# Optimization experiments

Measured on AMD Instinct MI355X. Metric: run time of the kernel, lower is better.

## Reference

```python
import math
import jax, jax.numpy as jnp
import numpy as np

TAU = 2.0 * math.pi
# First 32 imaginary parts of non-trivial zeta zeros (n_pairs = d_head//2 = 32)
RIEMANN_ZEROS_IM = (
    14.134725142, 21.022039639, 25.01085758, 30.424876126, 32.935061588,
    37.586178159, 40.918719012, 43.327073281, 48.005150881, 49.773832478,
    52.970321478, 56.446247697, 59.347044003, 60.831778525, 65.112544048,
    67.079810529, 69.546401711, 72.067157674, 75.704690699, 77.144840069,
    79.33737502, 82.910380854, 84.735492981, 87.425274613, 88.809111208,
    92.491899271, 94.651344041, 95.870634228, 98.831194218, 101.317851006,
    103.72553804, 105.446623052,
)

B, N, D_MODEL, N_HEADS = 2, 2048, 512, 8


def setup_inputs() -> dict:
    key = jax.random.key(0)
    k1, k2, k3 = jax.random.split(key, 3)
    d = D_MODEL
    x = jax.random.normal(k1, (B, N, d), dtype=jnp.float32)
    # scale weights ~ Xavier so attention logits stay in a sane range
    w_qkv = jax.random.normal(k2, (d, 3 * d), dtype=jnp.float32) * (d ** -0.5)
    w_o = jax.random.normal(k3, (d, d), dtype=jnp.float32) * (d ** -0.5)
    log_scale = jnp.zeros((N_HEADS,), dtype=jnp.float32)
    log_lambda_sigma = jnp.zeros((N_HEADS,), dtype=jnp.float32)
    return {"x": x, "w_qkv": w_qkv, "w_o": w_o,
            "log_scale": log_scale, "log_lambda_sigma": log_lambda_sigma}


def _rotate_pairs(t, cos, sin):
    # t: (B,H,N,dh); cos/sin: (H,N,K) with K = dh//2; rotate adjacent dim pairs
    t1 = t[..., 0::2]
    t2 = t[..., 1::2]
    c = cos[None]
    s = sin[None]
    r1 = t1 * c - t2 * s
    r2 = t1 * s + t2 * c
    return jnp.stack([r1, r2], axis=-1).reshape(t.shape)


def reference(x, w_qkv, w_o, log_scale, log_lambda_sigma):
    b, n, d_model = x.shape
    h = log_scale.shape[0]
    dh = d_model // h
    kpairs = dh // 2

    # qkv projection and head split
    qkv = (x @ w_qkv).reshape(b, n, 3, h, dh)
    q = jnp.transpose(qkv[:, :, 0], (0, 2, 1, 3))  # (B,H,N,dh)
    k = jnp.transpose(qkv[:, :, 1], (0, 2, 1, 3))
    v = jnp.transpose(qkv[:, :, 2], (0, 2, 1, 3))

    # phase theta(h,p,k) = log1p(p) * gamma_k * exp(log_scale_h)
    gamma = jnp.asarray(RIEMANN_ZEROS_IM[:kpairs], dtype=jnp.float32)
    gamma = gamma / gamma[0]  # normalize_gamma
    tau_t = jnp.log1p(jnp.arange(n, dtype=jnp.float32))
    theta = (tau_t[None, :, None] * gamma[None, None, :]
             * jnp.exp(log_scale)[:, None, None])  # (H,N,K)
    cos, sin = jnp.cos(theta), jnp.sin(theta)

    # sheet index sigma = floor(theta / 2pi); int cast in torch kills grad
    sheet = jax.lax.stop_gradient(jnp.floor(theta / TAU))  # (H,N,K) float

    # mean cross-pair |sigma_i - sigma_j|, accumulated over K via scan so the
    # (H,N,N,K) diff tensor never materializes (mirrors the module's tiling)
    def body(acc, sk):  # sk: (H,N)
        return acc + jnp.abs(sk[:, :, None] - sk[:, None, :]), None
    mean_abs, _ = jax.lax.scan(body, jnp.zeros((h, n, n), dtype=jnp.float32),
                               jnp.moveaxis(sheet, -1, 0))
    mean_abs = mean_abs / kpairs  # (H,N,N)

    lam = jnp.exp(log_lambda_sigma)  # (H,)
    sheet_bias = -lam[:, None, None] * mean_abs  # (H,N,N)
    causal = jnp.tril(jnp.ones((n, n), dtype=bool))
    bias = jnp.where(causal[None], sheet_bias, -jnp.inf)  # (H,N,N)

    q_rot = _rotate_pairs(q, cos, sin)
    k_rot = _rotate_pairs(k, cos, sin)

    scores = jnp.einsum("bhqd,bhkd->bhqk", q_rot, k_rot) / math.sqrt(dh)
    scores = scores + bias[None]
    attn = jax.nn.softmax(scores, axis=-1)
    out = jnp.einsum("bhqk,bhkd->bhqd", attn, v)
    out = jnp.transpose(out, (0, 2, 1, 3)).reshape(b, n, d_model)
    return out @ w_o
```

## Files before the change

kernel.cpp:

```cpp
#include <hip/hip_runtime.h>
#include <hip/hip_bf16.h>
#include <math.h>

#define NSEQ 2048
#define NH 8
#define DH 64
#define KP 32
#define DM 512
#define NB 2
#define MROWS (NB * NSEQ)
#define SLOT4 144

typedef short bf16x8 __attribute__((ext_vector_type(8)));
typedef float f32x4  __attribute__((ext_vector_type(4)));

static __constant__ float RZF[KP] = {
    14.134725142f, 21.022039639f, 25.01085758f,  30.424876126f, 32.935061588f,
    37.586178159f, 40.918719012f, 43.327073281f, 48.005150881f, 49.773832478f,
    52.970321478f, 56.446247697f, 59.347044003f, 60.831778525f, 65.112544048f,
    67.079810529f, 69.546401711f, 72.067157674f, 75.704690699f, 77.144840069f,
    79.33737502f,  82.910380854f, 84.735492981f, 87.425274613f, 88.809111208f,
    92.491899271f, 94.651344041f, 95.870634228f, 98.831194218f, 101.317851006f,
    103.72553804f, 105.446623052f};

static __device__ __forceinline__ unsigned short f2bf(float f) {
    unsigned int u = __float_as_uint(f);
    unsigned int r = (u + 0x7FFFu + ((u >> 16) & 1u)) >> 16;
    return (unsigned short)r;
}
static __device__ __forceinline__ float bf2f(unsigned short s) {
    return __uint_as_float((unsigned int)s << 16);
}

static __device__ __forceinline__ void gload16(const void* g, void* l) {
    __builtin_amdgcn_global_load_lds(
        (const __attribute__((address_space(1))) void*)g,
        (__attribute__((address_space(3))) void*)l, 16, 0, 0);
}

__global__ __launch_bounds__(256) void k_prep(
    const float* __restrict__ x, const float* __restrict__ wq,
    const float* __restrict__ wo, const float* __restrict__ ls,
    const float* __restrict__ ll,
    unsigned short* __restrict__ xb, unsigned short* __restrict__ wqT,
    unsigned short* __restrict__ woT,
    float* __restrict__ cosT, float* __restrict__ sinT, float* __restrict__ biasK)
{
    __shared__ float tile[32][33];
    int bid = blockIdx.x;
    int tid = threadIdx.x;
    if (bid < 1024) {
        int i = bid * 256 + tid;
        float4 a = ((const float4*)x)[2 * i];
        float4 b = ((const float4*)x)[2 * i + 1];
        union { unsigned short s[8]; uint4 u; } pk;
        pk.s[0] = f2bf(a.x); pk.s[1] = f2bf(a.y); pk.s[2] = f2bf(a.z); pk.s[3] = f2bf(a.w);
        pk.s[4] = f2bf(b.x); pk.s[5] = f2bf(b.y); pk.s[6] = f2bf(b.z); pk.s[7] = f2bf(b.w);
        ((uint4*)xb)[i] = pk.u;
    } else if (bid < 2048) {
        const float* src; unsigned short* dst; int R, C, bx, by;
        if (bid < 1792) { src = wq; dst = wqT; R = DM; C = 3 * DM;
                          int ix = bid - 1024; bx = ix % 48; by = ix / 48; }
        else            { src = wo; dst = woT; R = DM; C = DM;
                          int ix = bid - 1792; bx = ix & 15; by = ix >> 4; }
        int x0 = bx << 5, y0 = by << 5;
        int tx = tid & 31, ty = tid >> 5;
#pragma unroll
        for (int i = 0; i < 4; ++i)
            tile[ty + i * 8][tx] = src[(size_t)(y0 + ty + i * 8) * C + x0 + tx];
        __syncthreads();
#pragma unroll
        for (int i = 0; i < 4; ++i)
            dst[(size_t)(x0 + ty + i * 8) * R + y0 + tx] = f2bf(tile[tx][ty + i * 8]);
    } else {
        int item = (bid - 2048) * 256 + tid;
        int p   = item & 31;
        int idx = item >> 5;
        int h = idx >> 11;
        int t = idx & (NSEQ - 1);
        float scale = expf(ls[h]);
        float tau = log1pf((float)t);
        const float TAUF = 6.2831853071795864769f;
        float g  = RZF[p] / RZF[0];
        float th = (tau * g) * scale;
        cosT[(size_t)idx * KP + p] = cosf(th);
        sinT[(size_t)idx * KP + p] = sinf(th);
        float fl = floorf(th / TAUF);
        fl += __shfl_xor(fl, 1);
        fl += __shfl_xor(fl, 2);
        fl += __shfl_xor(fl, 4);
        fl += __shfl_xor(fl, 8);
        fl += __shfl_xor(fl, 16);
        if (p == 0) biasK[idx] = expf(ll[h]) * (1.0f / 32.0f) * fl;
    }
}

__global__ __launch_bounds__(256) void k_gemm_qkv(
    const unsigned short* __restrict__ xb, const unsigned short* __restrict__ wt,
    const float* __restrict__ cosT, const float* __restrict__ sinT,
    unsigned short* __restrict__ qrot, unsigned short* __restrict__ krot,
    unsigned short* __restrict__ vtout)
{
    __shared__ char Asm[2][64 * 128];
    __shared__ char Bsm[2][128 * 128];
    int tid = threadIdx.x;
    int w = tid >> 6, lane = tid & 63, g = lane >> 4, c = lane & 15;
    int wm = w >> 1, wn = w & 1;
    int bm = blockIdx.y << 6, bn = blockIdx.x << 7;
    int rin = lane >> 3;
    int csw = ((lane & 7) ^ rin) << 4;

    f32x4 acc[2][4];
#pragma unroll
    for (int mi = 0; mi < 2; ++mi)
#pragma unroll
        for (int ni = 0; ni < 4; ++ni) acc[mi][ni] = (f32x4){0.f, 0.f, 0.f, 0.f};

    const char* Ag = (const char*)xb;
    const char* Bg = (const char*)wt;

    auto stage = [&](int buf, int k0) {
#pragma unroll
        for (int ch = 0; ch < 2; ++ch) {
            int chA = w * 2 + ch;
            int row = chA * 8 + rin;
            gload16(Ag + ((size_t)(bm + row) * DM + k0) * 2 + csw, Asm[buf] + chA * 1024);
        }
#pragma unroll
        for (int ch = 0; ch < 4; ++ch) {
            int chB = w * 4 + ch;
            int row = chB * 8 + rin;
            gload16(Bg + ((size_t)(bn + row) * DM + k0) * 2 + csw, Bsm[buf] + chB * 1024);
        }
    };

    stage(0, 0);
    asm volatile("s_waitcnt vmcnt(0)" ::: "memory");
    __syncthreads();
    int cur = 0;

    for (int k0 = 0; k0 < DM; k0 += 64) {
        if (k0 + 64 < DM) stage(cur ^ 1, k0 + 64);
#pragma unroll
        for (int kk = 0; kk < 2; ++kk) {
            bf16x8 af[2], bfr[4];
#pragma unroll
            for (int mi = 0; mi < 2; ++mi) {
                int row = wm * 32 + mi * 16 + c;
                af[mi] = *(const bf16x8*)(Asm[cur] + ((row * 128 + kk * 64 + g * 16) ^ ((row & 7) << 4)));
            }
#pragma unroll
            for (int ni = 0; ni < 4; ++ni) {
                int row = wn * 64 + ni * 16 + c;
                bfr[ni] = *(const bf16x8*)(Bsm[cur] + ((row * 128 + kk * 64 + g * 16) ^ ((row & 7) << 4)));
            }
#pragma unroll
            for (int mi = 0; mi < 2; ++mi)
#pragma unroll
                for (int ni = 0; ni < 4; ++ni)
                    acc[mi][ni] = __builtin_amdgcn_mfma_f32_16x16x32_bf16(
                        af[mi], bfr[ni], acc[mi][ni], 0, 0, 0);
        }
        asm volatile("s_waitcnt vmcnt(0)" ::: "memory");
        __syncthreads();
        cur ^= 1;
    }

    int lane_odd = c & 1;
#pragma unroll
    for (int ni = 0; ni < 4; ++ni) {
        int n = bn + wn * 64 + ni * 16 + c;
        int sec = n >> 9;
        int dmod = n & 511;
        int h = dmod >> 6, dh = dmod & 63, p = dh >> 1;
        if (sec == 2) {
#pragma unroll
            for (int mi = 0; mi < 2; ++mi) {
                int m0 = bm + wm * 32 + mi * 16 + g * 4;
                int b = m0 >> 11, t0 = m0 & (NSEQ - 1);
                union { unsigned short s[4]; uint2 u; } pk;
                pk.s[0] = f2bf(acc[mi][ni][0]); pk.s[1] = f2bf(acc[mi][ni][1]);
                pk.s[2] = f2bf(acc[mi][ni][2]); pk.s[3] = f2bf(acc[mi][ni][3]);
                *(uint2*)(vtout + ((size_t)(b * NH + h) * DH + dh) * NSEQ + t0) = pk.u;
            }
        } else {
            const float* cb_ = cosT + (size_t)h * NSEQ * KP + p;
            const float* sb_ = sinT + (size_t)h * NSEQ * KP + p;
            unsigned short* dst = (sec == 0) ? qrot : krot;
            float osc = (sec == 0) ? 0.125f : 1.0f;
#pragma unroll
            for (int mi = 0; mi < 2; ++mi) {
#pragma unroll
                for (int r = 0; r < 4; ++r) {
                    int m = bm + wm * 32 + mi * 16 + g * 4 + r;
                    int b = m >> 11, t = m & (NSEQ - 1);
                    float val = acc[mi][ni][r];
                    float pv = __shfl_xor(val, 1);
                    float cv = cb_[(size_t)t * KP], sv = sb_[(size_t)t * KP];
                    float o = lane_odd ? (pv * sv + val * cv) : (val * cv - pv * sv);
                    dst[((size_t)(b * NH + h) * NSEQ + t) * DH + dh] = f2bf(o * osc);
                }
            }
        }
    }
}

__global__ __launch_bounds__(256) void k_attn(
    const unsigned short* __restrict__ qr, const unsigned short* __restrict__ kr,
    const unsigned short* __restrict__ vt, const float* __restrict__ biasK,
    unsigned short* __restrict__ ao, unsigned short* __restrict__ opart,
    float* __restrict__ mlpart)
{
    __shared__ char Kbuf[8192];
    __shared__ char Vbuf[8192];
    __shared__ char Pl[4][2048];
    __shared__ float Bk[64];

    int bid = blockIdx.x;
    int xcd = bid & 7;
    int i   = bid >> 3;
    int bh  = xcd * 2 + (i & 1);
    int slot = (SLOT4 - 1) - (i >> 1);
    int b = bh >> 3, h = bh & 7;
    int s = slot, qt = 0, nch;
    for (;;) { nch = (qt + 4) >> 2; if (s < nch) break; s -= nch; ++qt; }
    int ci = s;
    int t0 = ci << 2;
    int t1 = min(t0 + 4, qt + 1);

    int q0 = qt << 6;
    int tid = threadIdx.x;
    int w    = tid >> 6;
    int lane = tid & 63;
    int g    = lane >> 4;
    int c    = lane & 15;
    char* Pb = Pl[w];

    const char* kb  = (const char*)(kr + (size_t)bh * NSEQ * DH);
    const char* vtb = (const char*)(vt + (size_t)bh * DH * NSEQ);
    const unsigned short* qb = qr + (size_t)bh * NSEQ * DH;
    const float* bkrow = biasK + (size_t)h * NSEQ;

    int qg = q0 + (w << 4) + c;

    bf16x8 qf[2];
#pragma unroll
    for (int sl = 0; sl < 2; ++sl)
        qf[sl] = *(const bf16x8*)(qb + (size_t)qg * DH + sl * 32 + g * 8);

    f32x4 oa[4];
#pragma unroll
    for (int dt = 0; dt < 4; ++dt) oa[dt] = (f32x4){0.f, 0.f, 0.f, 0.f};
    float mr = -3.0e38f, lr = 0.0f;

    int rin = lane >> 3;
    int swz = ((lane & 7) ^ rin) << 4;

    for (int tile = t0; tile < t1; ++tile) {
        int j0 = tile << 6;
#pragma unroll
        for (int ii = 0; ii < 2; ++ii) {
            int ch = w * 2 + ii;
            int row = ch * 8 + rin;
            gload16(kb  + (size_t)(j0 + row) * 128 + swz, Kbuf + ch * 1024);
            gload16(vtb + (size_t)row * (NSEQ * 2) + (size_t)j0 * 2 + swz,
                    Vbuf + ch * 1024);
        }
        if (tid < 64) Bk[tid] = bkrow[j0 + tid];
        asm volatile("s_waitcnt vmcnt(0)" ::: "memory");
        __syncthreads();

        f32x4 st[4];
#pragma unroll
        for (int kt = 0; kt < 4; ++kt) st[kt] = (f32x4){0.f, 0.f, 0.f, 0.f};
#pragma unroll
        for (int sl = 0; sl < 2; ++sl) {
#pragma unroll
            for (int kt = 0; kt < 4; ++kt) {
                int row = kt * 16 + c;
                bf16x8 af = *(const bf16x8*)(Kbuf +
                    ((row * 128 + sl * 64 + g * 16) ^ ((row & 7) << 4)));
                st[kt] = __builtin_amdgcn_mfma_f32_16x16x32_bf16(af, qf[sl], st[kt], 0, 0, 0);
            }
        }

        bool diagT = (tile == qt);
        float sv[16];
#pragma unroll
        for (int kt = 0; kt < 4; ++kt) {
#pragma unroll
            for (int r4 = 0; r4 < 4; ++r4) {
                int ki = kt * 16 + g * 4 + r4;
                float vl = st[kt][r4] + Bk[ki];
                if (diagT && (j0 + ki > qg)) vl = -3.0e38f;
                sv[kt * 4 + r4] = vl;
            }
        }

        float m16 = sv[0];
#pragma unroll
        for (int ii = 1; ii < 16; ++ii) m16 = fmaxf(m16, sv[ii]);
        m16 = fmaxf(m16, __shfl_xor(m16, 16));
        m16 = fmaxf(m16, __shfl_xor(m16, 32));
        if (__any(m16 > mr + 8.0f)) {
            float mt = fmaxf(mr, m16);
            float corr = __expf(mr - mt);
            mr = mt;
            lr *= corr;
            float corrO[4];
#pragma unroll
            for (int r4 = 0; r4 < 4; ++r4) corrO[r4] = __shfl(corr, g * 4 + r4);
#pragma unroll
            for (int dt = 0; dt < 4; ++dt)
#pragma unroll
                for (int r4 = 0; r4 < 4; ++r4) oa[dt][r4] *= corrO[r4];
        }
        float psum = 0.0f;
        unsigned int pw[8];
#pragma unroll
        for (int ii = 0; ii < 8; ++ii) {
            float p0 = __expf(sv[2 * ii]     - mr);
            float p1 = __expf(sv[2 * ii + 1] - mr);
            psum += p0 + p1;
            asm("v_cvt_pk_bf16_f32 %0, %1, %2" : "=v"(pw[ii]) : "v"(p0), "v"(p1));
        }
        lr += psum;

#pragma unroll
        for (int kt = 0; kt < 4; ++kt) {
            uint2 u2; u2.x = pw[2 * kt]; u2.y = pw[2 * kt + 1];
            *(uint2*)(Pb + ((c * 128 + kt * 32 + g * 8) ^ ((c & 7) << 4))) = u2;
        }

#pragma unroll
        for (int sl = 0; sl < 2; ++sl) {
            bf16x8 pa = *(const bf16x8*)(Pb + ((c * 128 + sl * 64 + g * 16) ^ ((c & 7) << 4)));
#pragma unroll
            for (int dt = 0; dt < 4; ++dt) {
                int d = dt * 16 + c;
                bf16x8 vf = *(const bf16x8*)(Vbuf +
                    ((d * 128 + sl * 64 + g * 16) ^ ((d & 7) << 4)));
                oa[dt] = __builtin_amdgcn_mfma_f32_16x16x32_bf16(pa, vf, oa[dt], 0, 0, 0);
            }
        }
        __syncthreads();
    }

    lr += __shfl_xor(lr, 16);
    lr += __shfl_xor(lr, 32);
    if (nch == 1) {
        float inv = 1.0f / lr;
        float invO[4];
#pragma unroll
        for (int r4 = 0; r4 < 4; ++r4) invO[r4] = __shfl(inv, g * 4 + r4);
#pragma unroll
        for (int dt = 0; dt < 4; ++dt)
#pragma unroll
            for (int r4 = 0; r4 < 4; ++r4) {
                int row = q0 + (w << 4) + g * 4 + r4;
                ao[((size_t)b * NSEQ + row) * DM + h * DH + dt * 16 + c] =
                    f2bf(oa[dt][r4] * invO[r4]);
            }
    } else {
        size_t obase = ((size_t)bh * SLOT4 + slot) * (64 * 64);
#pragma unroll
        for (int dt = 0; dt < 4; ++dt)
#pragma unroll
            for (int r4 = 0; r4 < 4; ++r4) {
                int row = (w << 4) + g * 4 + r4;
                opart[obase + row * 64 + dt * 16 + c] = f2bf(oa[dt][r4]);
            }
        if (g == 0) {
            size_t mb = (((size_t)bh * SLOT4 + slot) * 64 + (w << 4) + c) * 2;
            mlpart[mb]     = mr;
            mlpart[mb + 1] = lr;
        }
    }
}

__global__ __launch_bounds__(256) void k_merge(
    const unsigned short* __restrict__ opart, const float* __restrict__ mlpart,
    unsigned short* __restrict__ ao)
{
    int bh = blockIdx.y;
    int b = bh >> 3, h = bh & 7;
    int qt = 4 + blockIdx.x;
    int nch = (qt + 4) >> 2;
    int slot0 = 0;
    for (int q = 0; q < qt; ++q) slot0 += (q + 4) >> 2;
    int tid = threadIdx.x;
    int row = tid >> 2;
    int d0 = (tid & 3) << 4;

    size_t pbase = ((size_t)bh * SLOT4 + slot0) * 4096 + row * 64 + d0;
    size_t mbase = (((size_t)bh * SLOT4 + slot0) * 64 + row) * 2;

    float M = -3.0e38f;
#pragma unroll
    for (int cc = 0; cc < 8; ++cc)
        if (cc < nch) M = fmaxf(M, mlpart[mbase + (size_t)cc * 128]);

    float L = 0.0f;
    float o[16];
#pragma unroll
    for (int ii = 0; ii < 16; ++ii) o[ii] = 0.0f;
#pragma unroll
    for (int cc = 0; cc < 8; ++cc) {
        if (cc < nch) {
            float mc = mlpart[mbase + (size_t)cc * 128];
            float lc = mlpart[mbase + (size_t)cc * 128 + 1];
            float wgt = __expf(mc - M);
            L += lc * wgt;
            union { uint4 u; unsigned short sh[8]; } lo, hi;
            lo.u = *(const uint4*)(opart + pbase + (size_t)cc * 4096);
            hi.u = *(const uint4*)(opart + pbase + (size_t)cc * 4096 + 8);
#pragma unroll
            for (int ii = 0; ii < 8; ++ii) {
                o[ii]     += bf2f(lo.sh[ii]) * wgt;
                o[ii + 8] += bf2f(hi.sh[ii]) * wgt;
            }
        }
    }
    float invL = 1.0f / L;
    int grow = (qt << 6) + row;
    unsigned short* dst = ao + ((size_t)b * NSEQ + grow) * DM + h * DH + d0;
    union { unsigned short sh[8]; uint4 u; } p0, p1;
#pragma unroll
    for (int ii = 0; ii < 8; ++ii) {
        p0.sh[ii] = f2bf(o[ii] * invL);
        p1.sh[ii] = f2bf(o[ii + 8] * invL);
    }
    *(uint4*)dst = p0.u;
    *(uint4*)(dst + 8) = p1.u;
}

__global__ __launch_bounds__(256) void k_gemm_out(
    const unsigned short* __restrict__ aob, const unsigned short* __restrict__ wt,
    float* __restrict__ out)
{
    __shared__ char Asm[64 * 128];
    __shared__ char Bsm[64 * 128];
    int tid = threadIdx.x;
    int w = tid >> 6, lane = tid & 63, g = lane >> 4, c = lane & 15;
    int wm = w >> 1, wn = w & 1;
    int bm = blockIdx.y << 6, bn = blockIdx.x << 6;
    int rin = lane >> 3;
    int csw = ((lane & 7) ^ rin) << 4;

    f32x4 acc[2][2];
#pragma unroll
    for (int mi = 0; mi < 2; ++mi)
#pragma unroll
        for (int ni = 0; ni < 2; ++ni) acc[mi][ni] = (f32x4){0.f, 0.f, 0.f, 0.f};

    const char* Ag = (const char*)aob;
    const char* Bg = (const char*)wt;

    for (int k0 = 0; k0 < DM; k0 += 64) {
        __syncthreads();
#pragma unroll
        for (int ch = 0; ch < 2; ++ch) {
            int chA = w * 2 + ch;
            int row = chA * 8 + rin;
            gload16(Ag + ((size_t)(bm + row) * DM + k0) * 2 + csw, Asm + chA * 1024);
        }
#pragma unroll
        for (int ch = 0; ch < 2; ++ch) {
            int chB = w * 2 + ch;
            int row = chB * 8 + rin;
            gload16(Bg + ((size_t)(bn + row) * DM + k0) * 2 + csw, Bsm + chB * 1024);
        }
        asm volatile("s_waitcnt vmcnt(0)" ::: "memory");
        __syncthreads();
#pragma unroll
        for (int kk = 0; kk < 2; ++kk) {
            bf16x8 af[2], bfr[2];
#pragma unroll
            for (int mi = 0; mi < 2; ++mi) {
                int row = wm * 32 + mi * 16 + c;
                af[mi] = *(const bf16x8*)(Asm + ((row * 128 + kk * 64 + g * 16) ^ ((row & 7) << 4)));
            }
#pragma unroll
            for (int ni = 0; ni < 2; ++ni) {
                int row = wn * 32 + ni * 16 + c;
                bfr[ni] = *(const bf16x8*)(Bsm + ((row * 128 + kk * 64 + g * 16) ^ ((row & 7) << 4)));
            }
#pragma unroll
            for (int mi = 0; mi < 2; ++mi)
#pragma unroll
                for (int ni = 0; ni < 2; ++ni)
                    acc[mi][ni] = __builtin_amdgcn_mfma_f32_16x16x32_bf16(
                        af[mi], bfr[ni], acc[mi][ni], 0, 0, 0);
        }
    }

#pragma unroll
    for (int ni = 0; ni < 2; ++ni) {
        int n = bn + wn * 32 + ni * 16 + c;
#pragma unroll
        for (int mi = 0; mi < 2; ++mi)
#pragma unroll
            for (int r = 0; r < 4; ++r) {
                int m = bm + wm * 32 + mi * 16 + g * 4 + r;
                out[(size_t)m * DM + n] = acc[mi][ni][r];
            }
    }
}

extern "C" void kernel_launch(void* const* d_in, const int* in_sizes, int n_in,
                              void* d_out, int out_size, void* d_ws, size_t ws_size,
                              hipStream_t stream)
{
    const float* x  = (const float*)d_in[0];
    const float* wq = (const float*)d_in[1];
    const float* wo = (const float*)d_in[2];
    const float* ls = (const float*)d_in[3];
    const float* ll = (const float*)d_in[4];
    float* out = (float*)d_out;

    char* ws = (char*)d_ws;
    size_t off = 0;
    float* cosT  = (float*)(ws + off); off += (size_t)NH * NSEQ * KP * 4;
    float* sinT  = (float*)(ws + off); off += (size_t)NH * NSEQ * KP * 4;
    float* biasK = (float*)(ws + off); off += (size_t)NH * NSEQ * 4;
    unsigned short* xb  = (unsigned short*)(ws + off); off += (size_t)MROWS * DM * 2;
    unsigned short* wqT = (unsigned short*)(ws + off); off += (size_t)DM * 3 * DM * 2;
    unsigned short* woT = (unsigned short*)(ws + off); off += (size_t)DM * DM * 2;
    unsigned short* qbf = (unsigned short*)(ws + off); off += (size_t)MROWS * DM * 2;
    unsigned short* kbf = (unsigned short*)(ws + off); off += (size_t)MROWS * DM * 2;
    unsigned short* vtb = (unsigned short*)(ws + off); off += (size_t)MROWS * DM * 2;
    unsigned short* aob = (unsigned short*)(ws + off); off += (size_t)MROWS * DM * 2;
    unsigned short* opart = (unsigned short*)(ws + off);
    off += (size_t)NB * NH * SLOT4 * 64 * 64 * 2;
    float* mlpart = (float*)(ws + off); off += (size_t)NB * NH * SLOT4 * 64 * 2 * 4;

    k_prep<<<4096, 256, 0, stream>>>(x, wq, wo, ls, ll, xb, wqT, woT, cosT, sinT, biasK);
    k_gemm_qkv<<<dim3(3 * DM / 128, MROWS / 64), 256, 0, stream>>>(
        xb, wqT, cosT, sinT, qbf, kbf, vtb);
    k_attn<<<8 * 288, 256, 0, stream>>>(
        qbf, kbf, vtb, biasK, aob, opart, mlpart);
    k_merge<<<dim3(28, NB * NH), 256, 0, stream>>>(opart, mlpart, aob);
    k_gemm_out<<<dim3(DM / 64, MROWS / 64), 256, 0, stream>>>(aob, woT, out);
}
```

Before: 71.07 us.

## Fold log2e into scores, use raw v_exp, load V directly into registers

Folds the log2(e) factor into the Q scaling and the sheet bias, so the softmax and merge steps can call the hardware base-2 exponential directly instead of __expf. V fragments are now loaded from global memory straight into registers, which removes the V shared-memory buffer and the LDS round trip. The kernel gets a launch-bounds occupancy hint, and the lazy-rescale threshold is raised to match the base-2 domain. In exchange, each wave now issues its own V global loads, which cost more bandwidth than the shared async copy did, and register pressure rises.

```diff
diff --git a/kernel.cpp b/kernel.cpp
--- a/kernel.cpp
+++ b/kernel.cpp
@@ -10,6 +10,7 @@
 #define NB 2
 #define MROWS (NB * NSEQ)
 #define SLOT4 144
+#define LOG2E 1.4426950408889634f
 
 typedef short bf16x8 __attribute__((ext_vector_type(8)));
 typedef float f32x4  __attribute__((ext_vector_type(4)));
@@ -30,6 +31,9 @@
 }
 static __device__ __forceinline__ float bf2f(unsigned short s) {
     return __uint_as_float((unsigned int)s << 16);
+}
+static __device__ __forceinline__ float exp2q(float x) {
+    float r; asm("v_exp_f32 %0, %1" : "=v"(r) : "v"(x)); return r;
 }
 
 static __device__ __forceinline__ void gload16(const void* g, void* l) {
@@ -91,7 +95,7 @@
         fl += __shfl_xor(fl, 4);
         fl += __shfl_xor(fl, 8);
         fl += __shfl_xor(fl, 16);
-        if (p == 0) biasK[idx] = expf(ll[h]) * (1.0f / 32.0f) * fl;
+        if (p == 0) biasK[idx] = expf(ll[h]) * (1.0f / 32.0f) * fl * LOG2E;
     }
 }
 
@@ -187,7 +191,7 @@
             const float* cb_ = cosT + (size_t)h * NSEQ * KP + p;
             const float* sb_ = sinT + (size_t)h * NSEQ * KP + p;
             unsigned short* dst = (sec == 0) ? qrot : krot;
-            float osc = (sec == 0) ? 0.125f : 1.0f;
+            float osc = (sec == 0) ? (0.125f * LOG2E) : 1.0f;
 #pragma unroll
             for (int mi = 0; mi < 2; ++mi) {
 #pragma unroll
@@ -205,14 +209,13 @@
     }
 }
 
-__global__ __launch_bounds__(256) void k_attn(
+__global__ __launch_bounds__(256, 4) void k_attn(
     const unsigned short* __restrict__ qr, const unsigned short* __restrict__ kr,
     const unsigned short* __restrict__ vt, const float* __restrict__ biasK,
     unsigned short* __restrict__ ao, unsigned short* __restrict__ opart,
     float* __restrict__ mlpart)
 {
     __shared__ char Kbuf[8192];
-    __shared__ char Vbuf[8192];
     __shared__ char Pl[4][2048];
     __shared__ float Bk[64];
 
@@ -262,11 +265,18 @@
         for (int ii = 0; ii < 2; ++ii) {
             int ch = w * 2 + ii;
             int row = ch * 8 + rin;
-            gload16(kb  + (size_t)(j0 + row) * 128 + swz, Kbuf + ch * 1024);
-            gload16(vtb + (size_t)row * (NSEQ * 2) + (size_t)j0 * 2 + swz,
-                    Vbuf + ch * 1024);
+            gload16(kb + (size_t)(j0 + row) * 128 + swz, Kbuf + ch * 1024);
         }
         if (tid < 64) Bk[tid] = bkrow[j0 + tid];
+        bf16x8 vr[2][4];
+#pragma unroll
+        for (int sl = 0; sl < 2; ++sl)
+#pragma unroll
+            for (int dt = 0; dt < 4; ++dt) {
+                int d = dt * 16 + c;
+                vr[sl][dt] = *(const bf16x8*)(vtb +
+                    (size_t)d * (NSEQ * 2) + j0 * 2 + sl * 64 + g * 16);
+            }
         asm volatile("s_waitcnt vmcnt(0)" ::: "memory");
         __syncthreads();
 
@@ -302,9 +312,9 @@
         for (int ii = 1; ii < 16; ++ii) m16 = fmaxf(m16, sv[ii]);
         m16 = fmaxf(m16, __shfl_xor(m16, 16));
         m16 = fmaxf(m16, __shfl_xor(m16, 32));
-        if (__any(m16 > mr + 8.0f)) {
+        if (__any(m16 > mr + 11.5f)) {
             float mt = fmaxf(mr, m16);
-            float corr = __expf(mr - mt);
+            float corr = exp2q(mr - mt);
             mr = mt;
             lr *= corr;
             float corrO[4];
@@ -319,8 +329,8 @@
         unsigned int pw[8];
 #pragma unroll
         for (int ii = 0; ii < 8; ++ii) {
-            float p0 = __expf(sv[2 * ii]     - mr);
-            float p1 = __expf(sv[2 * ii + 1] - mr);
+            float p0 = exp2q(sv[2 * ii]     - mr);
+            float p1 = exp2q(sv[2 * ii + 1] - mr);
             psum += p0 + p1;
             asm("v_cvt_pk_bf16_f32 %0, %1, %2" : "=v"(pw[ii]) : "v"(p0), "v"(p1));
         }
@@ -336,12 +346,8 @@
         for (int sl = 0; sl < 2; ++sl) {
             bf16x8 pa = *(const bf16x8*)(Pb + ((c * 128 + sl * 64 + g * 16) ^ ((c & 7) << 4)));
 #pragma unroll
-            for (int dt = 0; dt < 4; ++dt) {
-                int d = dt * 16 + c;
-                bf16x8 vf = *(const bf16x8*)(Vbuf +
-                    ((d * 128 + sl * 64 + g * 16) ^ ((d & 7) << 4)));
-                oa[dt] = __builtin_amdgcn_mfma_f32_16x16x32_bf16(pa, vf, oa[dt], 0, 0, 0);
-            }
+            for (int dt = 0; dt < 4; ++dt)
+                oa[dt] = __builtin_amdgcn_mfma_f32_16x16x32_bf16(pa, vr[sl][dt], oa[dt], 0, 0, 0);
         }
         __syncthreads();
     }
@@ -409,7 +415,7 @@
         if (cc < nch) {
             float mc = mlpart[mbase + (size_t)cc * 128];
             float lc = mlpart[mbase + (size_t)cc * 128 + 1];
-            float wgt = __expf(mc - M);
+            float wgt = exp2f(mc - M);
             L += lc * wgt;
             union { uint4 u; unsigned short sh[8]; } lo, hi;
             lo.u = *(const uint4*)(opart + pbase + (size_t)cc * 4096);
```

New measurement: 89.68 us. 1.26x slower.
